# Performance work log

Hardware: AMD Instinct MI355X
Metric: run time of the kernel (lower is better)

## Reference

```python
import jax, jax.numpy as jnp
import numpy as np

N_NODES = 20000
N_EDGES = 320000
NF = 128   # num_node_feats
EF = 32    # num_edge_feats
CF = 3     # num_coord_feats
H = 512    # hidden_dim


def setup_inputs() -> dict:
    key = jax.random.key(0)
    ks = jax.random.split(key, 20)
    s = lambda k, shape, fan_in: jax.random.normal(k, shape, jnp.float32) / np.sqrt(fan_in)
    return {
        "hfeats": jax.random.normal(ks[0], (N_NODES, NF), jnp.float32),
        "cfeats": jax.random.normal(ks[1], (N_NODES, CF), jnp.float32),
        "efeats": jax.random.normal(ks[2], (N_EDGES, EF), jnp.float32),
        "src": jax.random.randint(ks[3], (N_EDGES,), 0, N_NODES, jnp.int32),
        "dst": jax.random.randint(ks[4], (N_EDGES,), 0, N_NODES, jnp.int32),
        # node_expansion: Linear(NF, H)
        "Wn": s(ks[5], (NF, H), NF), "bn": jnp.zeros((H,), jnp.float32),
        # edge_expansion: Linear(EF, H)
        "We": s(ks[6], (EF, H), EF), "be": jnp.zeros((H,), jnp.float32),
        # coord_expansion: Linear(CF, H)
        "Wc": s(ks[7], (CF, H), CF), "bc": jnp.zeros((H,), jnp.float32),
        # combination_reduction_nfeats: Linear(H,H) -> CELU -> Linear(H,NF) -> CELU
        "Wn1": s(ks[8], (H, H), H), "bn1": jnp.zeros((H,), jnp.float32),
        "Wn2": s(ks[9], (H, NF), H), "bn2": jnp.zeros((NF,), jnp.float32),
        # combination_reduction_efeats: Linear(H, EF) -> CELU
        "Weo": s(ks[10], (H, EF), H), "beo": jnp.zeros((EF,), jnp.float32),
        # combination_reduction_cfeats: Linear(H, CF) -> CELU
        "Wco": s(ks[11], (H, CF), H), "bco": jnp.zeros((CF,), jnp.float32),
    }


def reference(hfeats, cfeats, efeats, src, dst,
              Wn, bn, We, be, Wc, bc,
              Wn1, bn1, Wn2, bn2, Weo, beo, Wco, bco):
    celu = jax.nn.celu
    n_nodes = hfeats.shape[0]
    # Feature expansions (Linear + CELU)
    h = celu(hfeats @ Wn + bn)   # [N, H]
    e = celu(efeats @ We + be)   # [E, H]
    c = celu(cfeats @ Wc + bc)   # [N, H]
    # edge_udf: x = |c_dst - c_src| * (h_src * e)   -> [E, H]
    x = jnp.abs(c[dst] - c[src]) * (h[src] * e)
    # update_all(copy_e, sum): scatter-sum edge messages to dst nodes
    k = jax.ops.segment_sum(x, dst, num_segments=n_nodes)  # [N, H]
    # Residual combination-reductions
    h_out = hfeats + celu(celu(k @ Wn1 + bn1) @ Wn2 + bn2)
    e_out = efeats + celu(e @ Weo + beo)
    c_out = cfeats + celu(c @ Wco + bco)
    return (h_out, c_out, e_out)
```

## Files before the change

kernel.cpp:

```cpp
#include <hip/hip_runtime.h>
#include <hip/hip_bf16.h>

#define NF 128
#define EF 32
#define CF 3
#define H  512
#define EB 32

typedef __attribute__((ext_vector_type(8))) short bf16x8;
typedef __attribute__((ext_vector_type(4))) float f32x4;

__device__ __forceinline__ float celu_f(float x) {
    return fmaxf(x, __expf(fminf(x, 0.0f)) - 1.0f);
}
__device__ __forceinline__ uint cvtpk(float lo, float hi) {
    uint r;
    asm("v_cvt_pk_bf16_f32 %0, %1, %2" : "=v"(r) : "v"(lo), "v"(hi));
    return r;
}
__device__ __forceinline__ bf16x8 pack8(float4 v0, float4 v1) {
    union { uint4 u; bf16x8 b; } r;
    r.u.x = cvtpk(v0.x, v0.y); r.u.y = cvtpk(v0.z, v0.w);
    r.u.z = cvtpk(v1.x, v1.y); r.u.w = cvtpk(v1.z, v1.w);
    return r.b;
}
__device__ __forceinline__ float b2f(ushort s) {
    union { uint u; float f; } v; v.u = ((uint)s) << 16; return v.f;
}
__device__ __forceinline__ void unpack4(uint2 v, float* o) {
    union { uint u; float f; } x;
    x.u = v.x << 16;          o[0] = x.f;
    x.u = v.x & 0xffff0000u;  o[1] = x.f;
    x.u = v.y << 16;          o[2] = x.f;
    x.u = v.y & 0xffff0000u;  o[3] = x.f;
}

__global__ void setup_kernel(const float* __restrict__ We, const float* __restrict__ Weo,
                             const float* __restrict__ Wn, const float* __restrict__ Wn1,
                             const float* __restrict__ Wn2, const int* __restrict__ dst,
                             ushort* __restrict__ Wet, ushort* __restrict__ Weot,
                             ushort* __restrict__ Wnt, ushort* __restrict__ Wn1t,
                             ushort* __restrict__ Wn2t, int* __restrict__ cnt,
                             float* __restrict__ k_buf, int n_edges, int nk4) {
    int i = blockIdx.x * 256 + threadIdx.x;
    if (i < H * EF) {
        int j = i / EF, k = i % EF;
        Wet[i] = (ushort)cvtpk(We[(size_t)k * H + j], 0.f);
        int o = i / H, j2 = i % H;
        Weot[i] = (ushort)cvtpk(Weo[(size_t)j2 * EF + o], 0.f);
    }
    if (i < H * NF) {
        int o = i >> 7, k = i & 127;
        Wnt[i] = (ushort)cvtpk(Wn[(size_t)k * H + o], 0.f);
        int o2 = i >> 9, k2 = i & 511;
        Wn2t[i] = (ushort)cvtpk(Wn2[(size_t)k2 * NF + o2], 0.f);
    }
    if (i < H * H) {
        int o = i >> 9, k = i & 511;
        Wn1t[i] = (ushort)cvtpk(Wn1[(size_t)k * H + o], 0.f);
    }
    const int nthreads = gridDim.x * 256;
    float4 z4 = {0.f, 0.f, 0.f, 0.f};
    for (int p = i; p < nk4; p += nthreads)
        ((float4*)k_buf)[p] = z4;
    for (int e = i; e < n_edges; e += nthreads)
        atomicAdd(&cnt[dst[e]], 1);
}

__global__ void scan_kernel(int* __restrict__ cnt, int n_nodes) {
    __shared__ int part[1024];
    const int t = threadIdx.x;
    const int per = (n_nodes + 1023) / 1024;
    int s = 0;
    for (int i = 0; i < per; ++i) {
        int idx = t * per + i;
        if (idx < n_nodes) s += cnt[idx];
    }
    part[t] = s;
    __syncthreads();
    for (int off = 1; off < 1024; off <<= 1) {
        int v = (t >= off) ? part[t - off] : 0;
        __syncthreads();
        part[t] += v;
        __syncthreads();
    }
    int acc = part[t] - s;
    for (int i = 0; i < per; ++i) {
        int idx = t * per + i;
        if (idx < n_nodes) {
            int c = cnt[idx];
            cnt[idx] = acc;
            acc += c;
        }
    }
}

__global__ __launch_bounds__(256) void node_expand_kernel(
        const float* __restrict__ hfeats, const float* __restrict__ cfeats,
        const ushort* __restrict__ Wnt, const float* __restrict__ bn,
        const float* __restrict__ Wc, const float* __restrict__ bc,
        ushort* __restrict__ hc, int n_nodes,
        const int* __restrict__ dst, int* __restrict__ cursor,
        int* __restrict__ perm, int n_edges, int nNE) {
    const int t = threadIdx.x;
    if (blockIdx.x >= nNE) {
        int i = (blockIdx.x - nNE) * 256 + t;
        if (i < n_edges) {
            int pos = atomicAdd(&cursor[dst[i]], 1);
            perm[pos] = i;
        }
        return;
    }
    __shared__ ushort hf[32 * NF];
    __shared__ float cf[32][4];
    const int lane = t & 63;
    const int w = t >> 6;
    const int node0 = blockIdx.x * 32;

    for (int i = t; i < 32 * 16; i += 256) {
        int row = i >> 4, g = i & 15;
        int node = node0 + row; if (node >= n_nodes) node = n_nodes - 1;
        const float* p = hfeats + (size_t)node * NF + g * 8;
        float4 v0 = *(const float4*)p;
        float4 v1 = *(const float4*)(p + 4);
        ((bf16x8*)hf)[row * 16 + (g ^ (row & 7))] = pack8(v0, v1);
    }
    for (int i = t; i < 32 * CF; i += 256) {
        int n = i / CF, k = i % CF;
        int node = node0 + n; if (node >= n_nodes) node = n_nodes - 1;
        cf[n][k] = cfeats[(size_t)node * CF + k];
    }
    __syncthreads();

    const int ar = lane & 15;
    const int hi = lane >> 4;
    const int ak = hi * 8;

    f32x4 acc[2][8];
    #pragma unroll
    for (int nt = 0; nt < 2; ++nt)
        #pragma unroll
        for (int q = 0; q < 8; ++q) { f32x4 z = {0.f,0.f,0.f,0.f}; acc[nt][q] = z; }

    for (int kstep = 0; kstep < NF / 32; ++kstep) {
        bf16x8 nfrag[2];
        #pragma unroll
        for (int nt = 0; nt < 2; ++nt) {
            int r = nt * 16 + ar;
            int g = kstep * 4 + hi;
            nfrag[nt] = ((const bf16x8*)hf)[r * 16 + (g ^ (r & 7))];
        }
        #pragma unroll
        for (int q = 0; q < 8; ++q) {
            bf16x8 wf = *(const bf16x8*)(Wnt + (size_t)((w * 8 + q) * 16 + ar) * NF + kstep * 32 + ak);
            acc[0][q] = __builtin_amdgcn_mfma_f32_16x16x32_bf16(wf, nfrag[0], acc[0][q], 0, 0, 0);
            acc[1][q] = __builtin_amdgcn_mfma_f32_16x16x32_bf16(wf, nfrag[1], acc[1][q], 0, 0, 0);
        }
    }
    #pragma unroll
    for (int q = 0; q < 8; ++q) {
        const int jbase = (w * 8 + q) * 16 + hi * 4;
        const float4 bv = *(const float4*)(bn + jbase);
        #pragma unroll
        for (int nt = 0; nt < 2; ++nt) {
            int node = node0 + nt * 16 + ar;
            if (node < n_nodes) {
                uint2 pk;
                pk.x = cvtpk(celu_f(acc[nt][q][0] + bv.x), celu_f(acc[nt][q][1] + bv.y));
                pk.y = cvtpk(celu_f(acc[nt][q][2] + bv.z), celu_f(acc[nt][q][3] + bv.w));
                *(uint2*)(hc + (size_t)node * 1024 + (jbase >> 2) * 8) = pk;
            }
        }
    }

    for (int i = t; i < 32 * 64; i += 256) {
        int n = i >> 6, gj = i & 63;
        int node = node0 + n;
        if (node < n_nodes) {
            int j = gj * 8;
            float c0 = cf[n][0], c1 = cf[n][1], c2 = cf[n][2];
            float v[8];
            #pragma unroll
            for (int u = 0; u < 8; ++u)
                v[u] = celu_f(bc[j + u] + c0 * Wc[j + u] + c1 * Wc[H + j + u] + c2 * Wc[2 * H + j + u]);
            uint2 p0, p1;
            p0.x = cvtpk(v[0], v[1]); p0.y = cvtpk(v[2], v[3]);
            p1.x = cvtpk(v[4], v[5]); p1.y = cvtpk(v[6], v[7]);
            *(uint2*)(hc + (size_t)node * 1024 + (2 * gj) * 8 + 4) = p0;
            *(uint2*)(hc + (size_t)node * 1024 + (2 * gj + 1) * 8 + 4) = p1;
        }
    }
}

__global__ __launch_bounds__(512, 4) void edge_kernel(
        const float* __restrict__ efeats,
        const int* __restrict__ src, const int* __restrict__ dst,
        const int* __restrict__ perm,
        const ushort* __restrict__ Wet, const float* __restrict__ be,
        const ushort* __restrict__ Weot, const float* __restrict__ beo,
        const ushort* __restrict__ hc,
        float* __restrict__ k_acc, float* __restrict__ e_out, int n_edges,
        int nEB,
        const float* __restrict__ cfeats, const float* __restrict__ Wco,
        const float* __restrict__ bco, float* __restrict__ c_out, int n_nodes) {
    const int t = threadIdx.x;
    const int lane = t & 63;
    const int w = t >> 6;

    if (blockIdx.x >= nEB) {
        const int node = (blockIdx.x - nEB) * 8 + w;
        if (node >= n_nodes) return;
        uint2 cv0 = *(const uint2*)(hc + (size_t)node * 1024 + (2 * lane) * 8 + 4);
        uint2 cv1 = *(const uint2*)(hc + (size_t)node * 1024 + (2 * lane + 1) * 8 + 4);
        float cv[8];
        unpack4(cv0, cv);
        unpack4(cv1, cv + 4);
        float a0 = 0.f, a1 = 0.f, a2 = 0.f;
        #pragma unroll
        for (int u = 0; u < 8; ++u) {
            int j = lane * 8 + u;
            a0 += cv[u] * Wco[j * CF + 0];
            a1 += cv[u] * Wco[j * CF + 1];
            a2 += cv[u] * Wco[j * CF + 2];
        }
        #pragma unroll
        for (int m = 32; m >= 1; m >>= 1) {
            a0 += __shfl_xor(a0, m);
            a1 += __shfl_xor(a1, m);
            a2 += __shfl_xor(a2, m);
        }
        if (lane < 3) {
            float s = (lane == 0) ? a0 : (lane == 1) ? a1 : a2;
            c_out[(size_t)node * CF + lane] = cfeats[(size_t)node * CF + lane] + celu_f(bco[lane] + s);
        }
        return;
    }

    __shared__ ushort e512[EB * 512];
    __shared__ int s_perm[EB], s_src[EB], s_dst[EB];

    const int q = nEB >> 3, r = nEB & 7;
    const int xcd = blockIdx.x & 7, sub = blockIdx.x >> 3;
    const int bid = (xcd < r ? xcd * (q + 1) : r * (q + 1) + (xcd - r) * q) + sub;
    const int e0 = bid * EB;

    if (t < EB) {
        int e = e0 + t;
        int pe = (e < n_edges) ? perm[e] : -1;
        s_perm[t] = pe;
        s_src[t] = (pe >= 0) ? src[pe] : 0;
        s_dst[t] = (pe >= 0) ? dst[pe] : -1;
    }
    __syncthreads();

    const int ar = lane & 15;
    const int hi = lane >> 4;
    const int ak = hi * 8;

    const int grp = t >> 7;
    const int ct = t & 127;
    const int j0 = ct * 4;
    const int g = j0 >> 3, go = j0 & 7;
    const int ebase = grp * 16;
    uint4 svb[2][4];
    uint2 cdb[2][4];
    uint2 evb[2][4];
    if (w < 4) {
        #pragma unroll
        for (int j = 0; j < 4; ++j) {
            const int e = ebase + j;
            const int s_ = s_src[e];
            int dc = s_dst[e]; dc = (dc < 0) ? 0 : dc;
            svb[0][j] = *(const uint4*)(hc + (size_t)s_ * 1024 + ct * 8);
            cdb[0][j] = *(const uint2*)(hc + (size_t)dc * 1024 + ct * 8 + 4);
        }
    }

    {
        bf16x8 wfrag[4];
        #pragma unroll
        for (int qq = 0; qq < 4; ++qq)
            wfrag[qq] = *(const bf16x8*)(Wet + (size_t)((w * 4 + qq) * 16 + ar) * EF + ak);
        #pragma unroll
        for (int et = 0; et < 2; ++et) {
            bf16x8 efrag;
            {
                int pe = s_perm[et * 16 + ar];
                if (pe < 0) pe = 0;
                const float* p = efeats + (size_t)pe * EF + ak;
                float4 v0 = *(const float4*)p;
                float4 v1 = *(const float4*)(p + 4);
                efrag = pack8(v0, v1);
            }
            f32x4 acc[4];
            #pragma unroll
            for (int qq = 0; qq < 4; ++qq) { f32x4 z = {0.f,0.f,0.f,0.f}; acc[qq] = z; }
            #pragma unroll
            for (int qq = 0; qq < 4; ++qq)
                acc[qq] = __builtin_amdgcn_mfma_f32_16x16x32_bf16(wfrag[qq], efrag, acc[qq], 0, 0, 0);
            const int e_l = et * 16 + ar;
            #pragma unroll
            for (int qq = 0; qq < 4; ++qq) {
                const int jbase = (w * 4 + qq) * 16 + hi * 4;
                const float4 bv = *(const float4*)(be + jbase);
                uint2 pk;
                pk.x = cvtpk(celu_f(acc[qq][0] + bv.x), celu_f(acc[qq][1] + bv.y));
                pk.y = cvtpk(celu_f(acc[qq][2] + bv.z), celu_f(acc[qq][3] + bv.w));
                const int gs = (jbase >> 3) ^ (e_l & 7);
                *(uint2*)(&e512[e_l * 512 + gs * 8 + (jbase & 7)]) = pk;
            }
        }
    }
    __syncthreads();

    if (w < 4) {
        float a_[4];
        a_[0] = a_[1] = a_[2] = a_[3] = 0.f;
        int cur = -1;

        #pragma unroll
        for (int j = 0; j < 4; ++j) {
            const int e = ebase + j;
            evb[0][j] = *(const uint2*)(&e512[e * 512 + (g ^ (e & 7)) * 8 + go]);
        }

        #pragma unroll
        for (int c = 0; c < 4; ++c) {
            const int cb = c & 1, nb = cb ^ 1;
            if (c < 3) {
                #pragma unroll
                for (int j = 0; j < 4; ++j) {
                    const int e = ebase + (c + 1) * 4 + j;
                    const int s_ = s_src[e];
                    int dc = s_dst[e]; dc = (dc < 0) ? 0 : dc;
                    svb[nb][j] = *(const uint4*)(hc + (size_t)s_ * 1024 + ct * 8);
                    cdb[nb][j] = *(const uint2*)(hc + (size_t)dc * 1024 + ct * 8 + 4);
                    evb[nb][j] = *(const uint2*)(&e512[e * 512 + (g ^ (e & 7)) * 8 + go]);
                }
            }
            #pragma unroll
            for (int j = 0; j < 4; ++j) {
                const int e = ebase + c * 4 + j;
                const int d = __builtin_amdgcn_readfirstlane(s_dst[e]);
                if (d != cur) {
                    if (cur >= 0) {
                        #pragma unroll
                        for (int u = 0; u < 4; ++u)
                            atomicAdd(&k_acc[(size_t)cur * H + j0 + u], a_[u]);
                        a_[0] = a_[1] = a_[2] = a_[3] = 0.f;
                    }
                    cur = d;
                }
                if (d >= 0) {
                    float hs_[4], cs_[4], cd_[4], ev_[4];
                    uint2 hv; hv.x = svb[cb][j].x; hv.y = svb[cb][j].y;
                    uint2 cv; cv.x = svb[cb][j].z; cv.y = svb[cb][j].w;
                    unpack4(hv, hs_);
                    unpack4(cv, cs_);
                    unpack4(cdb[cb][j], cd_);
                    unpack4(evb[cb][j], ev_);
                    #pragma unroll
                    for (int u = 0; u < 4; ++u)
                        a_[u] += fabsf(cd_[u] - cs_[u]) * (hs_[u] * ev_[u]);
                }
            }
        }
        if (cur >= 0) {
            #pragma unroll
            for (int u = 0; u < 4; ++u)
                atomicAdd(&k_acc[(size_t)cur * H + j0 + u], a_[u]);
        }
    } else {
        const int wc = w - 4;
        const int ot = wc & 1, et = wc >> 1;
        const int e_l = et * 16 + ar;
        f32x4 accc = {0.f, 0.f, 0.f, 0.f};
        #pragma unroll
        for (int kt = 0; kt < 16; ++kt) {
            bf16x8 wfC = *(const bf16x8*)(Weot + (size_t)(ot * 16 + ar) * H + kt * 32 + ak);
            const int gs = (kt * 4 + hi) ^ (e_l & 7);
            bf16x8 b = *(const bf16x8*)(&e512[e_l * 512 + gs * 8]);
            accc = __builtin_amdgcn_mfma_f32_16x16x32_bf16(wfC, b, accc, 0, 0, 0);
        }
        const int pe = s_perm[e_l];
        if (pe >= 0) {
            const int obase = ot * 16 + hi * 4;
            const float4 bo = *(const float4*)(beo + obase);
            size_t idx = (size_t)pe * EF + obase;
            float4 ef4 = *(const float4*)(efeats + idx);
            float4 o;
            o.x = ef4.x + celu_f(accc[0] + bo.x);
            o.y = ef4.y + celu_f(accc[1] + bo.y);
            o.z = ef4.z + celu_f(accc[2] + bo.z);
            o.w = ef4.w + celu_f(accc[3] + bo.w);
            *(float4*)(e_out + idx) = o;
        }
    }
}

__global__ __launch_bounds__(512, 4) void node_out_kernel(
        const float* __restrict__ hfeats, const float* __restrict__ k_acc,
        const ushort* __restrict__ Wn1t, const float* __restrict__ bn1,
        const ushort* __restrict__ Wn2t, const float* __restrict__ bn2,
        float* __restrict__ h_out, int n_nodes) {
    __shared__ ushort kt_s[64 * H];
    const int t = threadIdx.x;
    const int lane = t & 63;
    const int w = t >> 6;
    const int node0 = blockIdx.x * 64;

    for (int i = t; i < 64 * 64; i += 512) {
        int row = i >> 6, g = i & 63;
        int node = node0 + row; if (node >= n_nodes) node = n_nodes - 1;
        const float* p = k_acc + (size_t)node * H + g * 8;
        float4 v0 = *(const float4*)p;
        float4 v1 = *(const float4*)(p + 4);
        ((bf16x8*)kt_s)[row * 64 + (g ^ (row & 7))] = pack8(v0, v1);
    }
    __syncthreads();

    const int ar = lane & 15;
    const int hi = lane >> 4;
    const int ak = hi * 8;

    f32x4 acc[4][4];
    #pragma unroll
    for (int nt = 0; nt < 4; ++nt)
        #pragma unroll
        for (int q = 0; q < 4; ++q) { f32x4 z = {0.f,0.f,0.f,0.f}; acc[nt][q] = z; }

    for (int kstep = 0; kstep < H / 32; ++kstep) {
        bf16x8 kfrag[4];
        #pragma unroll
        for (int nt = 0; nt < 4; ++nt) {
            int rr = nt * 16 + ar;
            int g = kstep * 4 + hi;
            kfrag[nt] = ((const bf16x8*)kt_s)[rr * 64 + (g ^ (rr & 7))];
        }
        #pragma unroll
        for (int q = 0; q < 4; ++q) {
            bf16x8 wf = *(const bf16x8*)(Wn1t + (size_t)((w * 4 + q) * 16 + ar) * H + kstep * 32 + ak);
            #pragma unroll
            for (int nt = 0; nt < 4; ++nt)
                acc[nt][q] = __builtin_amdgcn_mfma_f32_16x16x32_bf16(wf, kfrag[nt], acc[nt][q], 0, 0, 0);
        }
    }
    __syncthreads();

    #pragma unroll
    for (int q = 0; q < 4; ++q) {
        const int jbase = (w * 4 + q) * 16 + hi * 4;
        const float4 bv = *(const float4*)(bn1 + jbase);
        #pragma unroll
        for (int nt = 0; nt < 4; ++nt) {
            const int rr = nt * 16 + ar;
            uint2 pk;
            pk.x = cvtpk(celu_f(acc[nt][q][0] + bv.x), celu_f(acc[nt][q][1] + bv.y));
            pk.y = cvtpk(celu_f(acc[nt][q][2] + bv.z), celu_f(acc[nt][q][3] + bv.w));
            const int gs = (jbase >> 3) ^ (rr & 7);
            *(uint2*)(&kt_s[rr * 512 + gs * 8 + (jbase & 7)]) = pk;
        }
    }
    __syncthreads();

    f32x4 acc2[4];
    #pragma unroll
    for (int nt = 0; nt < 4; ++nt) { f32x4 z = {0.f,0.f,0.f,0.f}; acc2[nt] = z; }

    for (int kstep = 0; kstep < H / 32; ++kstep) {
        bf16x8 wf = *(const bf16x8*)(Wn2t + (size_t)(w * 16 + ar) * H + kstep * 32 + ak);
        #pragma unroll
        for (int nt = 0; nt < 4; ++nt) {
            int rr = nt * 16 + ar;
            int g = kstep * 4 + hi;
            bf16x8 tfrag = ((const bf16x8*)kt_s)[rr * 64 + (g ^ (rr & 7))];
            acc2[nt] = __builtin_amdgcn_mfma_f32_16x16x32_bf16(wf, tfrag, acc2[nt], 0, 0, 0);
        }
    }
    {
        const int jbase = w * 16 + hi * 4;
        const float4 bv = *(const float4*)(bn2 + jbase);
        #pragma unroll
        for (int nt = 0; nt < 4; ++nt) {
            const int node = node0 + nt * 16 + ar;
            if (node < n_nodes) {
                size_t idx = (size_t)node * NF + jbase;
                float4 hf4 = *(const float4*)(hfeats + idx);
                float4 o;
                o.x = hf4.x + celu_f(acc2[nt][0] + bv.x);
                o.y = hf4.y + celu_f(acc2[nt][1] + bv.y);
                o.z = hf4.z + celu_f(acc2[nt][2] + bv.z);
                o.w = hf4.w + celu_f(acc2[nt][3] + bv.w);
                *(float4*)(h_out + idx) = o;
            }
        }
    }
}

extern "C" void kernel_launch(void* const* d_in, const int* in_sizes, int n_in,
                              void* d_out, int out_size, void* d_ws, size_t ws_size,
                              hipStream_t stream) {
    const float* hfeats = (const float*)d_in[0];
    const float* cfeats = (const float*)d_in[1];
    const float* efeats = (const float*)d_in[2];
    const int*   src    = (const int*)d_in[3];
    const int*   dst    = (const int*)d_in[4];
    const float* Wn  = (const float*)d_in[5];  const float* bn  = (const float*)d_in[6];
    const float* We  = (const float*)d_in[7];  const float* be  = (const float*)d_in[8];
    const float* Wc  = (const float*)d_in[9];  const float* bc  = (const float*)d_in[10];
    const float* Wn1 = (const float*)d_in[11]; const float* bn1 = (const float*)d_in[12];
    const float* Wn2 = (const float*)d_in[13]; const float* bn2 = (const float*)d_in[14];
    const float* Weo = (const float*)d_in[15]; const float* beo = (const float*)d_in[16];
    const float* Wco = (const float*)d_in[17]; const float* bco = (const float*)d_in[18];

    const int n_nodes = in_sizes[0] / NF;
    const int n_edges = in_sizes[2] / EF;

    float*  k_buf = (float*)d_ws;
    ushort* hc    = (ushort*)(k_buf + (size_t)n_nodes * H);
    ushort* Wet   = hc + (size_t)n_nodes * H * 2;
    ushort* Weot  = Wet + (size_t)H * EF;
    ushort* Wnt   = Weot + (size_t)H * EF;
    ushort* Wn1t  = Wnt + (size_t)H * NF;
    ushort* Wn2t  = Wn1t + (size_t)H * H;
    int*    cnt   = (int*)(Wn2t + (size_t)NF * H);
    int*    perm  = cnt + n_nodes;

    float* h_out = (float*)d_out;
    float* c_out = h_out + (size_t)n_nodes * NF;
    float* e_out = c_out + (size_t)n_nodes * CF;

    hipMemsetAsync(cnt, 0, (size_t)n_nodes * sizeof(int), stream);

    const int nk4 = (n_nodes * H) / 4;
    setup_kernel<<<(H * H + 255) / 256, 256, 0, stream>>>(
        We, Weo, Wn, Wn1, Wn2, dst, Wet, Weot, Wnt, Wn1t, Wn2t, cnt, k_buf,
        n_edges, nk4);

    scan_kernel<<<1, 1024, 0, stream>>>(cnt, n_nodes);

    const int nNE = (n_nodes + 31) / 32;
    const int nSC = (n_edges + 255) / 256;
    node_expand_kernel<<<nNE + nSC, 256, 0, stream>>>(
        hfeats, cfeats, Wnt, bn, Wc, bc, hc, n_nodes,
        dst, cnt, perm, n_edges, nNE);

    const int nEB = (n_edges + EB - 1) / EB;
    const int nCO = (n_nodes + 7) / 8;
    edge_kernel<<<nEB + nCO, 512, 0, stream>>>(
        efeats, src, dst, perm, Wet, be, Weot, beo, hc, k_buf, e_out, n_edges,
        nEB, cfeats, Wco, bco, c_out, n_nodes);

    node_out_kernel<<<(n_nodes + 63) / 64, 512, 0, stream>>>(
        hfeats, k_buf, Wn1t, bn1, Wn2t, bn2, h_out, n_nodes);
}
```

Before: 420.1 us.

## Process two edge tiles per block with ping-pong LDS and overlapped wave roles

Each edge-kernel block now handles two 32-edge tiles, each with its own LDS buffer. While waves 0-3 run the gather, multiply and atomic-scatter phase for the first tile, waves 4-7 compute that tile's e_out projection, build the second tile's expanded edge features and prefetch its gathers. The roles then swap for the second tile. The aim is to keep all waves busy and hide the edge-expansion and gather latency. The cost is double the shared memory per block, which may lower how many blocks fit on a CU.

```diff
diff --git a/kernel.cpp b/kernel.cpp
--- a/kernel.cpp
+++ b/kernel.cpp
@@ -200,15 +200,15 @@
         const ushort* __restrict__ Weot, const float* __restrict__ beo,
         const ushort* __restrict__ hc,
         float* __restrict__ k_acc, float* __restrict__ e_out, int n_edges,
-        int nEB,
+        int nEB2,
         const float* __restrict__ cfeats, const float* __restrict__ Wco,
         const float* __restrict__ bco, float* __restrict__ c_out, int n_nodes) {
     const int t = threadIdx.x;
     const int lane = t & 63;
     const int w = t >> 6;
 
-    if (blockIdx.x >= nEB) {
-        const int node = (blockIdx.x - nEB) * 8 + w;
+    if (blockIdx.x >= nEB2) {
+        const int node = (blockIdx.x - nEB2) * 8 + w;
         if (node >= n_nodes) return;
         uint2 cv0 = *(const uint2*)(hc + (size_t)node * 1024 + (2 * lane) * 8 + 4);
         uint2 cv1 = *(const uint2*)(hc + (size_t)node * 1024 + (2 * lane + 1) * 8 + 4);
@@ -236,15 +236,16 @@
         return;
     }
 
-    __shared__ ushort e512[EB * 512];
-    __shared__ int s_perm[EB], s_src[EB], s_dst[EB];
-
-    const int q = nEB >> 3, r = nEB & 7;
+    __shared__ ushort e512a[EB * 512];
+    __shared__ ushort e512b[EB * 512];
+    __shared__ int s_perm[2 * EB], s_src[2 * EB], s_dst[2 * EB];
+
+    const int q = nEB2 >> 3, r = nEB2 & 7;
     const int xcd = blockIdx.x & 7, sub = blockIdx.x >> 3;
     const int bid = (xcd < r ? xcd * (q + 1) : r * (q + 1) + (xcd - r) * q) + sub;
-    const int e0 = bid * EB;
-
-    if (t < EB) {
+    const int e0 = bid * (2 * EB);
+
+    if (t < 2 * EB) {
         int e = e0 + t;
         int pe = (e < n_edges) ? perm[e] : -1;
         s_perm[t] = pe;
@@ -256,19 +257,20 @@
     const int ar = lane & 15;
     const int hi = lane >> 4;
     const int ak = hi * 8;
-
-    const int grp = t >> 7;
-    const int ct = t & 127;
+    const int tt = t & 255;
+    const int grp = tt >> 7;
+    const int ct = tt & 127;
     const int j0 = ct * 4;
     const int g = j0 >> 3, go = j0 & 7;
-    const int ebase = grp * 16;
+
     uint4 svb[2][4];
     uint2 cdb[2][4];
     uint2 evb[2][4];
+
     if (w < 4) {
         #pragma unroll
         for (int j = 0; j < 4; ++j) {
-            const int e = ebase + j;
+            const int e = grp * 16 + j;
             const int s_ = s_src[e];
             int dc = s_dst[e]; dc = (dc < 0) ? 0 : dc;
             svb[0][j] = *(const uint4*)(hc + (size_t)s_ * 1024 + ct * 8);
@@ -276,72 +278,34 @@
         }
     }
 
-    {
-        bf16x8 wfrag[4];
-        #pragma unroll
-        for (int qq = 0; qq < 4; ++qq)
-            wfrag[qq] = *(const bf16x8*)(Wet + (size_t)((w * 4 + qq) * 16 + ar) * EF + ak);
-        #pragma unroll
-        for (int et = 0; et < 2; ++et) {
-            bf16x8 efrag;
-            {
-                int pe = s_perm[et * 16 + ar];
-                if (pe < 0) pe = 0;
-                const float* p = efeats + (size_t)pe * EF + ak;
-                float4 v0 = *(const float4*)p;
-                float4 v1 = *(const float4*)(p + 4);
-                efrag = pack8(v0, v1);
-            }
-            f32x4 acc[4];
-            #pragma unroll
-            for (int qq = 0; qq < 4; ++qq) { f32x4 z = {0.f,0.f,0.f,0.f}; acc[qq] = z; }
-            #pragma unroll
-            for (int qq = 0; qq < 4; ++qq)
-                acc[qq] = __builtin_amdgcn_mfma_f32_16x16x32_bf16(wfrag[qq], efrag, acc[qq], 0, 0, 0);
-            const int e_l = et * 16 + ar;
-            #pragma unroll
-            for (int qq = 0; qq < 4; ++qq) {
-                const int jbase = (w * 4 + qq) * 16 + hi * 4;
-                const float4 bv = *(const float4*)(be + jbase);
-                uint2 pk;
-                pk.x = cvtpk(celu_f(acc[qq][0] + bv.x), celu_f(acc[qq][1] + bv.y));
-                pk.y = cvtpk(celu_f(acc[qq][2] + bv.z), celu_f(acc[qq][3] + bv.w));
-                const int gs = (jbase >> 3) ^ (e_l & 7);
-                *(uint2*)(&e512[e_l * 512 + gs * 8 + (jbase & 7)]) = pk;
-            }
-        }
-    }
-    __syncthreads();
-
-    if (w < 4) {
+    auto runB = [&](const ushort* ebuf, const int tb) {
         float a_[4];
         a_[0] = a_[1] = a_[2] = a_[3] = 0.f;
         int cur = -1;
-
+        const int ebase = grp * 16;
         #pragma unroll
         for (int j = 0; j < 4; ++j) {
-            const int e = ebase + j;
-            evb[0][j] = *(const uint2*)(&e512[e * 512 + (g ^ (e & 7)) * 8 + go]);
-        }
-
+            const int el = ebase + j;
+            evb[0][j] = *(const uint2*)(&ebuf[el * 512 + (g ^ (el & 7)) * 8 + go]);
+        }
         #pragma unroll
         for (int c = 0; c < 4; ++c) {
             const int cb = c & 1, nb = cb ^ 1;
             if (c < 3) {
                 #pragma unroll
                 for (int j = 0; j < 4; ++j) {
-                    const int e = ebase + (c + 1) * 4 + j;
-                    const int s_ = s_src[e];
-                    int dc = s_dst[e]; dc = (dc < 0) ? 0 : dc;
+                    const int el = ebase + (c + 1) * 4 + j;
+                    const int s_ = s_src[tb + el];
+                    int dc = s_dst[tb + el]; dc = (dc < 0) ? 0 : dc;
                     svb[nb][j] = *(const uint4*)(hc + (size_t)s_ * 1024 + ct * 8);
                     cdb[nb][j] = *(const uint2*)(hc + (size_t)dc * 1024 + ct * 8 + 4);
-                    evb[nb][j] = *(const uint2*)(&e512[e * 512 + (g ^ (e & 7)) * 8 + go]);
+                    evb[nb][j] = *(const uint2*)(&ebuf[el * 512 + (g ^ (el & 7)) * 8 + go]);
                 }
             }
             #pragma unroll
             for (int j = 0; j < 4; ++j) {
-                const int e = ebase + c * 4 + j;
-                const int d = __builtin_amdgcn_readfirstlane(s_dst[e]);
+                const int el = ebase + c * 4 + j;
+                const int d = __builtin_amdgcn_readfirstlane(s_dst[tb + el]);
                 if (d != cur) {
                     if (cur >= 0) {
                         #pragma unroll
@@ -370,19 +334,20 @@
             for (int u = 0; u < 4; ++u)
                 atomicAdd(&k_acc[(size_t)cur * H + j0 + u], a_[u]);
         }
-    } else {
-        const int wc = w - 4;
+    };
+
+    auto runC = [&](const ushort* ebuf, const int tb, const int wc) {
         const int ot = wc & 1, et = wc >> 1;
-        const int e_l = et * 16 + ar;
+        const int el = et * 16 + ar;
         f32x4 accc = {0.f, 0.f, 0.f, 0.f};
         #pragma unroll
         for (int kt = 0; kt < 16; ++kt) {
             bf16x8 wfC = *(const bf16x8*)(Weot + (size_t)(ot * 16 + ar) * H + kt * 32 + ak);
-            const int gs = (kt * 4 + hi) ^ (e_l & 7);
-            bf16x8 b = *(const bf16x8*)(&e512[e_l * 512 + gs * 8]);
+            const int gs = (kt * 4 + hi) ^ (el & 7);
+            bf16x8 b = *(const bf16x8*)(&ebuf[el * 512 + gs * 8]);
             accc = __builtin_amdgcn_mfma_f32_16x16x32_bf16(wfC, b, accc, 0, 0, 0);
         }
-        const int pe = s_perm[e_l];
+        const int pe = s_perm[tb + el];
         if (pe >= 0) {
             const int obase = ot * 16 + hi * 4;
             const float4 bo = *(const float4*)(beo + obase);
@@ -395,6 +360,83 @@
             o.w = ef4.w + celu_f(accc[3] + bo.w);
             *(float4*)(e_out + idx) = o;
         }
+    };
+
+    {
+        bf16x8 wfrag[4];
+        #pragma unroll
+        for (int qq = 0; qq < 4; ++qq)
+            wfrag[qq] = *(const bf16x8*)(Wet + (size_t)((w * 4 + qq) * 16 + ar) * EF + ak);
+        #pragma unroll
+        for (int et = 0; et < 2; ++et) {
+            int pe = s_perm[et * 16 + ar];
+            if (pe < 0) pe = 0;
+            const float* p = efeats + (size_t)pe * EF + ak;
+            bf16x8 efrag = pack8(*(const float4*)p, *(const float4*)(p + 4));
+            f32x4 acc[4];
+            #pragma unroll
+            for (int qq = 0; qq < 4; ++qq) { f32x4 z = {0.f,0.f,0.f,0.f}; acc[qq] = z; }
+            #pragma unroll
+            for (int qq = 0; qq < 4; ++qq)
+                acc[qq] = __builtin_amdgcn_mfma_f32_16x16x32_bf16(wfrag[qq], efrag, acc[qq], 0, 0, 0);
+            const int el = et * 16 + ar;
+            #pragma unroll
+            for (int qq = 0; qq < 4; ++qq) {
+                const int jbase = (w * 4 + qq) * 16 + hi * 4;
+                const float4 bv = *(const float4*)(be + jbase);
+                uint2 pk;
+                pk.x = cvtpk(celu_f(acc[qq][0] + bv.x), celu_f(acc[qq][1] + bv.y));
+                pk.y = cvtpk(celu_f(acc[qq][2] + bv.z), celu_f(acc[qq][3] + bv.w));
+                const int gs = (jbase >> 3) ^ (el & 7);
+                *(uint2*)(&e512a[el * 512 + gs * 8 + (jbase & 7)]) = pk;
+            }
+        }
+    }
+    __syncthreads();
+
+    if (w < 4) {
+        runB(e512a, 0);
+    } else {
+        runC(e512a, 0, w - 4);
+        {
+            const int wa = w - 4;
+            #pragma unroll
+            for (int et = 0; et < 2; ++et) {
+                int pe = s_perm[32 + et * 16 + ar];
+                if (pe < 0) pe = 0;
+                const float* p = efeats + (size_t)pe * EF + ak;
+                bf16x8 efrag = pack8(*(const float4*)p, *(const float4*)(p + 4));
+                const int el = et * 16 + ar;
+                #pragma unroll
+                for (int qq = 0; qq < 8; ++qq) {
+                    bf16x8 wf = *(const bf16x8*)(Wet + (size_t)((wa * 8 + qq) * 16 + ar) * EF + ak);
+                    f32x4 acc = {0.f, 0.f, 0.f, 0.f};
+                    acc = __builtin_amdgcn_mfma_f32_16x16x32_bf16(wf, efrag, acc, 0, 0, 0);
+                    const int jbase = (wa * 8 + qq) * 16 + hi * 4;
+                    const float4 bv = *(const float4*)(be + jbase);
+                    uint2 pk;
+                    pk.x = cvtpk(celu_f(acc[0] + bv.x), celu_f(acc[1] + bv.y));
+                    pk.y = cvtpk(celu_f(acc[2] + bv.z), celu_f(acc[3] + bv.w));
+                    const int gs = (jbase >> 3) ^ (el & 7);
+                    *(uint2*)(&e512b[el * 512 + gs * 8 + (jbase & 7)]) = pk;
+                }
+            }
+        }
+        #pragma unroll
+        for (int j = 0; j < 4; ++j) {
+            const int e = 32 + grp * 16 + j;
+            const int s_ = s_src[e];
+            int dc = s_dst[e]; dc = (dc < 0) ? 0 : dc;
+            svb[0][j] = *(const uint4*)(hc + (size_t)s_ * 1024 + ct * 8);
+            cdb[0][j] = *(const uint2*)(hc + (size_t)dc * 1024 + ct * 8 + 4);
+        }
+    }
+    __syncthreads();
+
+    if (w >= 4) {
+        runB(e512b, 32);
+    } else {
+        runC(e512b, 32, w);
     }
 }
 
@@ -545,11 +587,12 @@
         hfeats, cfeats, Wnt, bn, Wc, bc, hc, n_nodes,
         dst, cnt, perm, n_edges, nNE);
 
-    const int nEB = (n_edges + EB - 1) / EB;
+    const int nT = (n_edges + EB - 1) / EB;
+    const int nEB2 = (nT + 1) / 2;
     const int nCO = (n_nodes + 7) / 8;
-    edge_kernel<<<nEB + nCO, 512, 0, stream>>>(
+    edge_kernel<<<nEB2 + nCO, 512, 0, stream>>>(
         efeats, src, dst, perm, Wet, be, Weot, beo, hc, k_buf, e_out, n_edges,
-        nEB, cfeats, Wco, bco, c_out, n_nodes);
+        nEB2, cfeats, Wco, bco, c_out, n_nodes);
 
     node_out_kernel<<<(n_nodes + 63) / 64, 512, 0, stream>>>(
         hfeats, k_buf, Wn1t, bn1, Wn2t, bn2, h_out, n_nodes);
```

After: 447.5 us. 1.07x slower.
